# Kernel tuning notes

Hardware: AMD Instinct MI355X
Metric: run time of the kernel (lower is better)

The kernel has to match this reference:

```python
import jax, jax.numpy as jnp
import numpy as np

B, S, E, H = 1, 8192, 1024, 16
D = E // H
SEG_LENS = [2048, 4096, 8192]
DILATIONS = [1, 2, 4]


def setup_inputs() -> dict:
    key = jax.random.key(0)
    k0, k1, k2 = jax.random.split(key, 3)
    sc_in = 1.0 / np.sqrt(E)
    return {
        "x": jax.random.normal(k0, (B, S, E), jnp.float32),
        "w_qkv": jax.random.normal(k1, (3 * E, E), jnp.float32) * sc_in,
        "b_qkv": jnp.zeros((3 * E,), jnp.float32),
        "w_out": jax.random.normal(k2, (E, E), jnp.float32) * sc_in,
        "b_out": jnp.zeros((E,), jnp.float32),
    }


def _sdpa(q, k, v):
    # q,k,v: [B,H,N,D]; standard scaled dot-product attention (non-causal)
    scale = 1.0 / np.sqrt(q.shape[-1])
    scores = jnp.einsum('bhqd,bhkd->bhqk', q, k) * scale
    probs = jax.nn.softmax(scores, axis=-1)
    return jnp.einsum('bhqk,bhkd->bhqd', probs, v)


def reference(x, w_qkv, b_qkv, w_out, b_out):
    # QKV projection: torch Linear is x @ W^T + b
    qkv = x @ w_qkv.T + b_qkv                       # [B,S,3E]
    qkv = qkv.reshape(B, S, 3, H, D).transpose(2, 0, 3, 1, 4)  # [3,B,H,S,D]
    q, k, v = qkv[0], qkv[1], qkv[2]

    seg_outputs = []
    for seg_len, dil in zip(SEG_LENS, DILATIONS):
        if seg_len > S:
            continue
        if dil > 1:
            n = min(seg_len, S // dil)
            pos = np.arange(0, n * dil, dil)        # strided dilated gather
        else:
            pos = np.arange(seg_len)                # leading segment
        o = _sdpa(q[:, :, pos], k[:, :, pos], v[:, :, pos])
        # scatter back to full length (zero elsewhere); also handles zero-padding
        full = jnp.zeros((B, H, S, D), x.dtype).at[:, :, pos, :].set(o)
        seg_outputs.append(full)

    if len(seg_outputs) == 0:
        out = jnp.zeros((B, H, S, D), x.dtype)
    else:
        out = seg_outputs[0]
        for so in seg_outputs[1:]:
            out = out + so
        out = out / len(seg_outputs)                # stack(...).mean(0)

    out = out.transpose(0, 2, 1, 3).reshape(B, S, E)
    return out @ w_out.T + b_out
```

## Files before the change

kernel.cpp:

```cpp
#include <hip/hip_runtime.h>


typedef __attribute__((ext_vector_type(8))) short bf16x8;
typedef __attribute__((ext_vector_type(4))) float f32x4;

#define MFMA(a, b, c) __builtin_amdgcn_mfma_f32_16x16x32_bf16((a), (b), (c), 0, 0, 0)

#if __has_builtin(__builtin_amdgcn_exp2f)
#define EXP2(x) __builtin_amdgcn_exp2f(x)
#else
#define EXP2(x) exp2f(x)
#endif

static __device__ __forceinline__ unsigned short f2bf(float f) {
  unsigned int u = __float_as_uint(f);
  unsigned int r = (u + 0x7FFFu + ((u >> 16) & 1u)) >> 16;
  return (unsigned short)r;
}

__global__ void cvt_f32_bf16(const float* __restrict__ in,
                             unsigned short* __restrict__ out, int n8) {
  int i = blockIdx.x * blockDim.x + threadIdx.x;
  if (i >= n8) return;
  const float4* p = (const float4*)in + (size_t)i * 2;
  float4 a = p[0];
  float4 b = p[1];
  union { bf16x8 v; unsigned short u[8]; } o;
  o.u[0] = f2bf(a.x); o.u[1] = f2bf(a.y); o.u[2] = f2bf(a.z); o.u[3] = f2bf(a.w);
  o.u[4] = f2bf(b.x); o.u[5] = f2bf(b.y); o.u[6] = f2bf(b.z); o.u[7] = f2bf(b.w);
  *((bf16x8*)out + i) = o.v;
}

template <int EPILOGUE>
__global__ __launch_bounds__(256, 2) void gemm_bt(
    const unsigned short* __restrict__ A, const unsigned short* __restrict__ B,
    const float* __restrict__ bias, void* __restrict__ Cout, int N, int K) {
  __shared__ unsigned short At[128 * 32];
  __shared__ unsigned short Bt[128 * 32];
  const int tid = threadIdx.x;
  const int wave = tid >> 6, lane = tid & 63;
  const int quad = lane >> 4, lc = lane & 15;
  const int wm = (wave >> 1) * 64, wn = (wave & 1) * 64;
  const int m0 = blockIdx.x * 128, n0 = blockIdx.y * 128;

  f32x4 acc[4][4] = {};

  for (int k0 = 0; k0 < K; k0 += 32) {
    __syncthreads();
#pragma unroll
    for (int issue = 0; issue < 2; ++issue) {
      const int cbase = issue * 256 + wave * 64;
      const int c = cbase + lane;
      const int row = c >> 2, col8 = (c & 3) * 8;
      __builtin_amdgcn_global_load_lds(
          (const __attribute__((address_space(1))) void*)&A[(size_t)(m0 + row) * K + k0 + col8],
          (__attribute__((address_space(3))) void*)&At[cbase * 8], 16, 0, 0);
      __builtin_amdgcn_global_load_lds(
          (const __attribute__((address_space(1))) void*)&B[(size_t)(n0 + row) * K + k0 + col8],
          (__attribute__((address_space(3))) void*)&Bt[cbase * 8], 16, 0, 0);
    }
    __syncthreads();
    bf16x8 af[4], bfr[4];
#pragma unroll
    for (int t = 0; t < 4; ++t)
      af[t] = *(const bf16x8*)&At[(wm + t * 16 + lc) * 32 + quad * 8];
#pragma unroll
    for (int t = 0; t < 4; ++t)
      bfr[t] = *(const bf16x8*)&Bt[(wn + t * 16 + lc) * 32 + quad * 8];
#pragma unroll
    for (int i = 0; i < 4; ++i)
#pragma unroll
      for (int j = 0; j < 4; ++j)
        acc[i][j] = MFMA(af[i], bfr[j], acc[i][j]);
  }

#pragma unroll
  for (int i = 0; i < 4; ++i) {
#pragma unroll
    for (int j = 0; j < 4; ++j) {
      const int gcol = n0 + wn + j * 16 + lc;
      const float bs = bias[gcol];
#pragma unroll
      for (int r = 0; r < 4; ++r) {
        const int grow = m0 + wm + i * 16 + quad * 4 + r;
        const float v = acc[i][j][r] + bs;
        if (EPILOGUE == 0) {
          const int which = gcol >> 10, rem = gcol & 1023;
          const int hh = rem >> 6, d = rem & 63;
          const float vs = (which == 0) ? v * 0.18033688f : v;
          ((unsigned short*)Cout)[(((size_t)(which * 16 + hh)) * 8192 + grow) * 64 + d] = f2bf(vs);
        } else {
          ((float*)Cout)[(size_t)grow * N + gcol] = v;
        }
      }
    }
  }
}

__global__ void transpose_v(const unsigned short* __restrict__ v,
                            unsigned short* __restrict__ vt1,
                            unsigned short* __restrict__ vt2,
                            unsigned short* __restrict__ vt3) {
  __shared__ unsigned short Tt[64 * 72];
  const int tid = threadIdx.x;
  const int h = blockIdx.y;
  const int bx = blockIdx.x;
  const unsigned short* src = v + (size_t)h * 8192 * 64;
  unsigned short* dst;
  int dil, Nk, t0;
  if (bx < 32)      { dst = vt1; dil = 1; Nk = 2048; t0 = bx; }
  else if (bx < 96) { dst = vt2; dil = 2; Nk = 4096; t0 = bx - 32; }
  else              { dst = vt3; dil = 4; Nk = 2048; t0 = bx - 96; }
  dst += (size_t)h * 64 * Nk;
  const int j0 = t0 * 64;
#pragma unroll
  for (int it = 0; it < 2; ++it) {
    const int slot = tid + it * 256;
    const int jj = slot >> 3, c8 = (slot & 7) * 8;
    *(bf16x8*)&Tt[jj * 72 + c8] =
        *(const bf16x8*)&src[(size_t)(j0 + jj) * dil * 64 + c8];
  }
  __syncthreads();
  const int d = tid >> 2, pg = (tid & 3) * 16;
  union { bf16x8 v2[2]; unsigned short u[16]; } ob;
#pragma unroll
  for (int t = 0; t < 16; ++t) {
    const int pos = pg + t;
    const int jj = (pos & 3) * 16 + (pos >> 2);
    ob.u[t] = Tt[jj * 72 + d];
  }
  *(bf16x8*)&dst[(size_t)d * Nk + j0 + pg] = ob.v2[0];
  *(bf16x8*)&dst[(size_t)d * Nk + j0 + pg + 8] = ob.v2[1];
}

__global__ __launch_bounds__(256, 2) void flash_all(
    const unsigned short* __restrict__ qkvb,
    const unsigned short* __restrict__ vt1, float* __restrict__ o1,
    const unsigned short* __restrict__ vt2, float* __restrict__ o2,
    const unsigned short* __restrict__ vt3, float* __restrict__ o3) {
  __shared__ unsigned short Kt[64 * 72];
  __shared__ unsigned short Vt[80 * 72];
  __shared__ unsigned short Pt[4][32 * 72];

  const int z = blockIdx.z;
  const int Nk = (z == 1) ? 4096 : 2048;
  const int qt = blockIdx.x;
  if (qt * 128 >= Nk) return;
  const int dil = 1 << z;
  const unsigned short* vt = (z == 0) ? vt1 : (z == 1) ? vt2 : vt3;
  float* o = (z == 0) ? o1 : (z == 1) ? o2 : o3;

  const int tid = threadIdx.x;
  const int wave = tid >> 6, lane = tid & 63;
  const int quad = lane >> 4, lc = lane & 15;
  const int h = blockIdx.y;

  const unsigned short* qh = qkvb + (size_t)h * 8192 * 64;
  const unsigned short* kh = qkvb + (size_t)(16 + h) * 8192 * 64;
  const unsigned short* vh = vt + (size_t)h * 64 * Nk;

  {
    const int r = 64 + (tid >> 4), c4 = (tid & 15) * 4;
    *(unsigned long long*)&Vt[r * 72 + c4] = 0x3F803F803F803F80ull;
  }

  bf16x8 qf[2][2];
#pragma unroll
  for (int mb = 0; mb < 2; ++mb) {
    const int qrow = qt * 128 + wave * 32 + mb * 16 + lc;
    qf[mb][0] = *(const bf16x8*)&qh[(size_t)qrow * dil * 64 + quad * 8];
    qf[mb][1] = *(const bf16x8*)&qh[(size_t)qrow * dil * 64 + quad * 8 + 32];
  }

  __syncthreads();
  const bf16x8 vone0 = *(const bf16x8*)&Vt[(64 + lc) * 72 + quad * 8];
  const bf16x8 vone1 = *(const bf16x8*)&Vt[(64 + lc) * 72 + quad * 8 + 32];

  f32x4 oacc[2][4] = {};
  f32x4 lacc[2] = {};

  const int srow = tid >> 3, scol8 = (tid & 7) * 8;

  bf16x8 kg0 = *(const bf16x8*)&kh[(size_t)srow * dil * 64 + scol8];
  bf16x8 kg1 = *(const bf16x8*)&kh[(size_t)(srow + 32) * dil * 64 + scol8];
  bf16x8 vg0 = *(const bf16x8*)&vh[(size_t)srow * Nk + scol8];
  bf16x8 vg1 = *(const bf16x8*)&vh[(size_t)(srow + 32) * Nk + scol8];

  for (int kb = 0; kb < Nk; kb += 64) {
    __syncthreads();
    *(bf16x8*)&Kt[srow * 72 + scol8] = kg0;
    *(bf16x8*)&Kt[(srow + 32) * 72 + scol8] = kg1;
    *(bf16x8*)&Vt[srow * 72 + scol8] = vg0;
    *(bf16x8*)&Vt[(srow + 32) * 72 + scol8] = vg1;
    __syncthreads();

    if (kb + 64 < Nk) {
      const int nk = kb + 64;
      kg0 = *(const bf16x8*)&kh[(size_t)(nk + srow) * dil * 64 + scol8];
      kg1 = *(const bf16x8*)&kh[(size_t)(nk + srow + 32) * dil * 64 + scol8];
      vg0 = *(const bf16x8*)&vh[(size_t)srow * Nk + nk + scol8];
      vg1 = *(const bf16x8*)&vh[(size_t)(srow + 32) * Nk + nk + scol8];
    }

    f32x4 sacc[2][4] = {};
#pragma unroll
    for (int jb = 0; jb < 4; ++jb) {
      const bf16x8 b0 = *(const bf16x8*)&Kt[(jb * 16 + lc) * 72 + quad * 8];
      const bf16x8 b1 = *(const bf16x8*)&Kt[(jb * 16 + lc) * 72 + quad * 8 + 32];
#pragma unroll
      for (int mb = 0; mb < 2; ++mb) {
        sacc[mb][jb] = MFMA(qf[mb][0], b0, sacc[mb][jb]);
        sacc[mb][jb] = MFMA(qf[mb][1], b1, sacc[mb][jb]);
      }
    }

#pragma unroll
    for (int mb = 0; mb < 2; ++mb)
#pragma unroll
      for (int jb = 0; jb < 4; ++jb)
#pragma unroll
        for (int r = 0; r < 4; ++r) sacc[mb][jb][r] = EXP2(sacc[mb][jb][r]);

#pragma unroll
    for (int mb = 0; mb < 2; ++mb)
#pragma unroll
      for (int r = 0; r < 4; ++r) {
        const unsigned int a0 = __float_as_uint(sacc[mb][0][r]) + 0x8000u;
        const unsigned int a1 = __float_as_uint(sacc[mb][1][r]) + 0x8000u;
        const unsigned int a2 = __float_as_uint(sacc[mb][2][r]) + 0x8000u;
        const unsigned int a3 = __float_as_uint(sacc[mb][3][r]) + 0x8000u;
        uint2 w;
        w.x = __builtin_amdgcn_perm(a1, a0, 0x07060302u);
        w.y = __builtin_amdgcn_perm(a3, a2, 0x07060302u);
        *(uint2*)&Pt[wave][(mb * 16 + quad * 4 + r) * 72 + lc * 4] = w;
      }

    bf16x8 pf[2][2];
#pragma unroll
    for (int mb = 0; mb < 2; ++mb) {
      pf[mb][0] = *(const bf16x8*)&Pt[wave][(mb * 16 + lc) * 72 + quad * 8];
      pf[mb][1] = *(const bf16x8*)&Pt[wave][(mb * 16 + lc) * 72 + quad * 8 + 32];
    }
#pragma unroll
    for (int nb = 0; nb < 4; ++nb) {
      const bf16x8 v0 = *(const bf16x8*)&Vt[(nb * 16 + lc) * 72 + quad * 8];
      const bf16x8 v1 = *(const bf16x8*)&Vt[(nb * 16 + lc) * 72 + quad * 8 + 32];
#pragma unroll
      for (int mb = 0; mb < 2; ++mb) {
        oacc[mb][nb] = MFMA(pf[mb][0], v0, oacc[mb][nb]);
        oacc[mb][nb] = MFMA(pf[mb][1], v1, oacc[mb][nb]);
      }
    }
#pragma unroll
    for (int mb = 0; mb < 2; ++mb) {
      lacc[mb] = MFMA(pf[mb][0], vone0, lacc[mb]);
      lacc[mb] = MFMA(pf[mb][1], vone1, lacc[mb]);
    }
  }

#pragma unroll
  for (int mb = 0; mb < 2; ++mb)
#pragma unroll
    for (int r = 0; r < 4; ++r) {
      const int row = wave * 32 + mb * 16 + quad * 4 + r;
      const float inv = 1.0f / (3.0f * lacc[mb][r]);
      const size_t base = (size_t)(qt * 128 + row) * 1024 + h * 64;
#pragma unroll
      for (int nb = 0; nb < 4; ++nb)
        o[base + nb * 16 + lc] = oacc[mb][nb][r] * inv;
    }
}

__global__ void combine(const float* __restrict__ o1, const float* __restrict__ o2,
                        const float* __restrict__ o3,
                        unsigned short* __restrict__ a3b) {
  const int idx = blockIdx.x * 256 + threadIdx.x;
  const int s = idx >> 7, e = (idx & 127) * 8;
  float acc[8] = {};
  if (s < 2048) {
    const float4* p = (const float4*)&o1[(size_t)s * 1024 + e];
#pragma unroll
    for (int t = 0; t < 4; ++t) { acc[t] += ((const float*)p)[t]; acc[4 + t] += ((const float*)p)[4 + t]; }
  }
  if (!(s & 1)) {
    const float4* p = (const float4*)&o2[(size_t)(s >> 1) * 1024 + e];
#pragma unroll
    for (int t = 0; t < 4; ++t) { acc[t] += ((const float*)p)[t]; acc[4 + t] += ((const float*)p)[4 + t]; }
  }
  if (!(s & 3)) {
    const float4* p = (const float4*)&o3[(size_t)(s >> 2) * 1024 + e];
#pragma unroll
    for (int t = 0; t < 4; ++t) { acc[t] += ((const float*)p)[t]; acc[4 + t] += ((const float*)p)[4 + t]; }
  }
  union { bf16x8 v; unsigned short u[8]; } ob;
#pragma unroll
  for (int t = 0; t < 8; ++t) ob.u[t] = f2bf(acc[t]);
  *(bf16x8*)&a3b[(size_t)s * 1024 + e] = ob.v;
}

extern "C" void kernel_launch(void* const* d_in, const int* in_sizes, int n_in,
                              void* d_out, int out_size, void* d_ws, size_t ws_size,
                              hipStream_t stream) {
  const float* x     = (const float*)d_in[0];
  const float* w_qkv = (const float*)d_in[1];
  const float* b_qkv = (const float*)d_in[2];
  const float* w_out = (const float*)d_in[3];
  const float* b_out = (const float*)d_in[4];
  float* out = (float*)d_out;

  char* ws = (char*)d_ws;
  unsigned short* qkvb  = (unsigned short*)(ws);
  float*          o1    = (float*)(ws + 33554432);
  float*          o3    = (float*)(ws + 41943040);
  unsigned short* vt1   = (unsigned short*)(ws + 50331648);
  unsigned short* vt2   = (unsigned short*)(ws + 54525952);
  unsigned short* vt3   = (unsigned short*)(ws + 62914560);
  float*          o2    = (float*)(ws + 67108864);
  unsigned short* wqkvb = (unsigned short*)(ws + 83886080);
  unsigned short* woutb = (unsigned short*)(ws + 90177536);
  unsigned short* xb    = (unsigned short*)(ws + 92274688);
  unsigned short* a3b   = xb;

  cvt_f32_bf16<<<dim3(8388608 / 8 / 256), dim3(256), 0, stream>>>(x, xb, 8388608 / 8);
  cvt_f32_bf16<<<dim3(3145728 / 8 / 256), dim3(256), 0, stream>>>(w_qkv, wqkvb, 3145728 / 8);
  cvt_f32_bf16<<<dim3(1048576 / 8 / 256), dim3(256), 0, stream>>>(w_out, woutb, 1048576 / 8);

  gemm_bt<0><<<dim3(64, 24), dim3(256), 0, stream>>>(xb, wqkvb, b_qkv, qkvb, 3072, 1024);

  transpose_v<<<dim3(128, 16), dim3(256), 0, stream>>>(qkvb + (size_t)32 * 8192 * 64,
                                                       vt1, vt2, vt3);

  flash_all<<<dim3(32, 16, 3), dim3(256), 0, stream>>>(qkvb, vt1, o1, vt2, o2, vt3, o3);

  combine<<<dim3(4096), dim3(256), 0, stream>>>(o1, o2, o3, a3b);

  gemm_bt<1><<<dim3(64, 8), dim3(256), 0, stream>>>(a3b, woutb, b_out, out, 1024, 1024);
}
```

Measured before the change: 357.9 us.

## Load K/V fragments directly from global memory, dropping LDS staging and block syncs

The flash attention kernel no longer stages K and V tiles through shared memory. Each wave now reads its MFMA B-operand fragments straight from global memory (served by L2/L1), which removes two block-wide barriers per key block and the software register prefetch. The all-ones bf16 vector for the row-sum MFMA is now built in registers, and the launch bounds go from 2 to 4 blocks per CU to use the freed LDS. The cost is redundant global traffic, since every wave re-reads the same K/V rows, plus exposed load latency without explicit prefetch. The dilated K rows are also strided, so cache locality is poorer.

```diff
diff --git a/kernel.cpp b/kernel.cpp
--- a/kernel.cpp
+++ b/kernel.cpp
@@ -133,13 +133,11 @@
   *(bf16x8*)&dst[(size_t)d * Nk + j0 + pg + 8] = ob.v2[1];
 }
 
-__global__ __launch_bounds__(256, 2) void flash_all(
+__global__ __launch_bounds__(256, 4) void flash_all(
     const unsigned short* __restrict__ qkvb,
     const unsigned short* __restrict__ vt1, float* __restrict__ o1,
     const unsigned short* __restrict__ vt2, float* __restrict__ o2,
     const unsigned short* __restrict__ vt3, float* __restrict__ o3) {
-  __shared__ unsigned short Kt[64 * 72];
-  __shared__ unsigned short Vt[80 * 72];
   __shared__ unsigned short Pt[4][32 * 72];
 
   const int z = blockIdx.z;
@@ -159,11 +157,6 @@
   const unsigned short* kh = qkvb + (size_t)(16 + h) * 8192 * 64;
   const unsigned short* vh = vt + (size_t)h * 64 * Nk;
 
-  {
-    const int r = 64 + (tid >> 4), c4 = (tid & 15) * 4;
-    *(unsigned long long*)&Vt[r * 72 + c4] = 0x3F803F803F803F80ull;
-  }
-
   bf16x8 qf[2][2];
 #pragma unroll
   for (int mb = 0; mb < 2; ++mb) {
@@ -172,41 +165,24 @@
     qf[mb][1] = *(const bf16x8*)&qh[(size_t)qrow * dil * 64 + quad * 8 + 32];
   }
 
-  __syncthreads();
-  const bf16x8 vone0 = *(const bf16x8*)&Vt[(64 + lc) * 72 + quad * 8];
-  const bf16x8 vone1 = *(const bf16x8*)&Vt[(64 + lc) * 72 + quad * 8 + 32];
+  union { bf16x8 v; unsigned short u[8]; } one_u;
+#pragma unroll
+  for (int t = 0; t < 8; ++t) one_u.u[t] = 0x3F80;
+  const bf16x8 vone = one_u.v;
 
   f32x4 oacc[2][4] = {};
   f32x4 lacc[2] = {};
 
-  const int srow = tid >> 3, scol8 = (tid & 7) * 8;
-
-  bf16x8 kg0 = *(const bf16x8*)&kh[(size_t)srow * dil * 64 + scol8];
-  bf16x8 kg1 = *(const bf16x8*)&kh[(size_t)(srow + 32) * dil * 64 + scol8];
-  bf16x8 vg0 = *(const bf16x8*)&vh[(size_t)srow * Nk + scol8];
-  bf16x8 vg1 = *(const bf16x8*)&vh[(size_t)(srow + 32) * Nk + scol8];
+  const unsigned short* kbase = kh + (size_t)lc * dil * 64 + quad * 8;
+  const unsigned short* vbase = vh + (size_t)lc * Nk + quad * 8;
 
   for (int kb = 0; kb < Nk; kb += 64) {
-    __syncthreads();
-    *(bf16x8*)&Kt[srow * 72 + scol8] = kg0;
-    *(bf16x8*)&Kt[(srow + 32) * 72 + scol8] = kg1;
-    *(bf16x8*)&Vt[srow * 72 + scol8] = vg0;
-    *(bf16x8*)&Vt[(srow + 32) * 72 + scol8] = vg1;
-    __syncthreads();
-
-    if (kb + 64 < Nk) {
-      const int nk = kb + 64;
-      kg0 = *(const bf16x8*)&kh[(size_t)(nk + srow) * dil * 64 + scol8];
-      kg1 = *(const bf16x8*)&kh[(size_t)(nk + srow + 32) * dil * 64 + scol8];
-      vg0 = *(const bf16x8*)&vh[(size_t)srow * Nk + nk + scol8];
-      vg1 = *(const bf16x8*)&vh[(size_t)(srow + 32) * Nk + nk + scol8];
-    }
-
     f32x4 sacc[2][4] = {};
 #pragma unroll
     for (int jb = 0; jb < 4; ++jb) {
-      const bf16x8 b0 = *(const bf16x8*)&Kt[(jb * 16 + lc) * 72 + quad * 8];
-      const bf16x8 b1 = *(const bf16x8*)&Kt[(jb * 16 + lc) * 72 + quad * 8 + 32];
+      const unsigned short* kr = kbase + (size_t)(kb + jb * 16) * dil * 64;
+      const bf16x8 b0 = *(const bf16x8*)kr;
+      const bf16x8 b1 = *(const bf16x8*)(kr + 32);
 #pragma unroll
       for (int mb = 0; mb < 2; ++mb) {
         sacc[mb][jb] = MFMA(qf[mb][0], b0, sacc[mb][jb]);
@@ -241,10 +217,12 @@
       pf[mb][0] = *(const bf16x8*)&Pt[wave][(mb * 16 + lc) * 72 + quad * 8];
       pf[mb][1] = *(const bf16x8*)&Pt[wave][(mb * 16 + lc) * 72 + quad * 8 + 32];
     }
+
 #pragma unroll
     for (int nb = 0; nb < 4; ++nb) {
-      const bf16x8 v0 = *(const bf16x8*)&Vt[(nb * 16 + lc) * 72 + quad * 8];
-      const bf16x8 v1 = *(const bf16x8*)&Vt[(nb * 16 + lc) * 72 + quad * 8 + 32];
+      const unsigned short* vr = vbase + (size_t)nb * 16 * Nk + kb;
+      const bf16x8 v0 = *(const bf16x8*)vr;
+      const bf16x8 v1 = *(const bf16x8*)(vr + 32);
 #pragma unroll
       for (int mb = 0; mb < 2; ++mb) {
         oacc[mb][nb] = MFMA(pf[mb][0], v0, oacc[mb][nb]);
@@ -253,8 +231,8 @@
     }
 #pragma unroll
     for (int mb = 0; mb < 2; ++mb) {
-      lacc[mb] = MFMA(pf[mb][0], vone0, lacc[mb]);
-      lacc[mb] = MFMA(pf[mb][1], vone1, lacc[mb]);
+      lacc[mb] = MFMA(pf[mb][0], vone, lacc[mb]);
+      lacc[mb] = MFMA(pf[mb][1], vone, lacc[mb]);
     }
   }
 
```

New measurement: 649.5 us. +81.5%, slower.
